# Kernel optimization log

Hardware: AMD Instinct MI355X
Metric: run time of the kernel (lower is better)

Reference implementation:

```python
import jax, jax.numpy as jnp
import numpy as np

N_NODES = 10000
N_EDGES = 160000
N_GRAPHS = 100
D = 32
E_DIM = 6
Q = 96
C = 2
EPS = 1e-5
S2S_STEPS = 3


def _bn(x, gamma, beta):
    # BatchNorm1d in training mode: normalize over the batch (row) axis
    mu = jnp.mean(x, axis=0)
    var = jnp.var(x, axis=0)
    return gamma * (x - mu) * jax.lax.rsqrt(var + EPS) + beta


def _mlp_layer(x, w, b, gamma, beta):
    # Linear -> ReLU -> BatchNorm1d (one block of the MLP helper)
    return _bn(jax.nn.relu(x @ w.T + b), gamma, beta)


def _nnconv(x, src, dst, edge_attr, nw, nb, ng, nbeta, root, bias):
    # edge MLP -> per-edge [D, D] weight matrices
    w = _mlp_layer(edge_attr, nw, nb, ng, nbeta).reshape(-1, D, D)  # [E, D, D]
    msg = jnp.einsum('ei,eio->eo', x[src], w)                       # per-edge matvec
    agg = jax.ops.segment_sum(msg, dst, num_segments=N_NODES)      # aggr='add'
    return agg + x @ root + bias                                    # root weight + bias


def _set2set(x, batch, w_ih, w_hh, b_ih, b_hh):
    h = jnp.zeros((N_GRAPHS, Q), x.dtype)
    c = jnp.zeros((N_GRAPHS, Q), x.dtype)
    q_star = jnp.zeros((N_GRAPHS, 2 * Q), x.dtype)
    for _ in range(S2S_STEPS):
        gates = q_star @ w_ih.T + b_ih + h @ w_hh.T + b_hh  # [B, 4Q], gate order i,f,g,o
        i, f, g, o = jnp.split(gates, 4, axis=1)
        c = jax.nn.sigmoid(f) * c + jax.nn.sigmoid(i) * jnp.tanh(g)
        h = jax.nn.sigmoid(o) * jnp.tanh(c)
        e = jnp.sum(x * h[batch], axis=-1)  # [N] attention logits
        emax = jax.ops.segment_max(e, batch, num_segments=N_GRAPHS)
        emax = jnp.where(jnp.isfinite(emax), emax, 0.0)
        a = jnp.exp(e - emax[batch])
        asum = jax.ops.segment_sum(a, batch, num_segments=N_GRAPHS)
        a = a / asum[batch]
        r = jax.ops.segment_sum(a[:, None] * x, batch, num_segments=N_GRAPHS)  # [B, Q]
        q_star = jnp.concatenate([h, r], axis=1)
    return q_star  # [B, 2Q]


def setup_inputs() -> dict:
    key = jax.random.key(0)
    ks = iter(jax.random.split(key, 48))
    def rn(shape, fan_in):
        return jax.random.normal(next(ks), shape, dtype=jnp.float32) * (1.0 / np.sqrt(fan_in))
    d = {}
    d['x'] = jax.random.normal(next(ks), (N_NODES, D), dtype=jnp.float32)
    d['edge_attr'] = jax.random.uniform(next(ks), (N_EDGES, E_DIM), dtype=jnp.float32)
    # conv1 edge-MLP + root + bias
    d['c1_nn_w'] = rn((D * D, E_DIM), E_DIM); d['c1_nn_b'] = jnp.zeros((D * D,), jnp.float32)
    d['c1_nn_g'] = jnp.ones((D * D,), jnp.float32); d['c1_nn_beta'] = jnp.zeros((D * D,), jnp.float32)
    d['c1_root'] = rn((D, D), D); d['c1_bias'] = jnp.zeros((D,), jnp.float32)
    # conv2
    d['c2_nn_w'] = rn((D * D, E_DIM), E_DIM); d['c2_nn_b'] = jnp.zeros((D * D,), jnp.float32)
    d['c2_nn_g'] = jnp.ones((D * D,), jnp.float32); d['c2_nn_beta'] = jnp.zeros((D * D,), jnp.float32)
    d['c2_root'] = rn((D, D), D); d['c2_bias'] = jnp.zeros((D,), jnp.float32)
    # lin1: MLP([2D, Q])
    d['lin1_w'] = rn((Q, 2 * D), 2 * D); d['lin1_b'] = jnp.zeros((Q,), jnp.float32)
    d['lin1_g'] = jnp.ones((Q,), jnp.float32); d['lin1_beta'] = jnp.zeros((Q,), jnp.float32)
    # Set2Set LSTM: input 2Q -> hidden Q
    d['lstm_w_ih'] = rn((4 * Q, 2 * Q), 2 * Q); d['lstm_w_hh'] = rn((4 * Q, Q), Q)
    d['lstm_b_ih'] = jnp.zeros((4 * Q,), jnp.float32); d['lstm_b_hh'] = jnp.zeros((4 * Q,), jnp.float32)
    # S2Slin: Linear(2Q, Q)
    d['s2s_w'] = rn((Q, 2 * Q), 2 * Q); d['s2s_b'] = jnp.zeros((Q,), jnp.float32)
    # mlp1: MLP([Q, Q, C])
    d['m1_w'] = rn((Q, Q), Q); d['m1_b'] = jnp.zeros((Q,), jnp.float32)
    d['m1_g'] = jnp.ones((Q,), jnp.float32); d['m1_beta'] = jnp.zeros((Q,), jnp.float32)
    d['m2_w'] = rn((C, Q), Q); d['m2_b'] = jnp.zeros((C,), jnp.float32)
    d['m2_g'] = jnp.ones((C,), jnp.float32); d['m2_beta'] = jnp.zeros((C,), jnp.float32)
    # graph structure
    d['edge_src'] = jax.random.randint(next(ks), (N_EDGES,), 0, N_NODES, dtype=jnp.int32)
    d['edge_dst'] = jax.random.randint(next(ks), (N_EDGES,), 0, N_NODES, dtype=jnp.int32)
    d['batch'] = jnp.sort(jax.random.randint(next(ks), (N_NODES,), 0, N_GRAPHS, dtype=jnp.int32))
    return d


def reference(x, edge_attr,
              c1_nn_w, c1_nn_b, c1_nn_g, c1_nn_beta, c1_root, c1_bias,
              c2_nn_w, c2_nn_b, c2_nn_g, c2_nn_beta, c2_root, c2_bias,
              lin1_w, lin1_b, lin1_g, lin1_beta,
              lstm_w_ih, lstm_w_hh, lstm_b_ih, lstm_b_hh,
              s2s_w, s2s_b,
              m1_w, m1_b, m1_g, m1_beta,
              m2_w, m2_b, m2_g, m2_beta,
              edge_src, edge_dst, batch):
    x1 = _nnconv(x, edge_src, edge_dst, edge_attr, c1_nn_w, c1_nn_b, c1_nn_g, c1_nn_beta, c1_root, c1_bias)
    x2 = _nnconv(x1, edge_src, edge_dst, edge_attr, c2_nn_w, c2_nn_b, c2_nn_g, c2_nn_beta, c2_root, c2_bias)
    xc = _mlp_layer(jnp.concatenate([x1, x2], axis=1), lin1_w, lin1_b, lin1_g, lin1_beta)  # [N, Q]
    qs = _set2set(xc, batch, lstm_w_ih, lstm_w_hh, lstm_b_ih, lstm_b_hh)                   # [B, 2Q]
    xg = qs @ s2s_w.T + s2s_b                                                               # [B, Q]
    xg = _mlp_layer(xg, m1_w, m1_b, m1_g, m1_beta)
    out = _mlp_layer(xg, m2_w, m2_b, m2_g, m2_beta)                                         # [B, C]
    return out
```

## Files before the change

### kernel.cpp

```cpp
#include <hip/hip_runtime.h>
#include <math.h>

#define NN 10000
#define NE 160000
#define NG 100
#define DD 32
#define QQ 96
#define EPS 1e-5f

typedef float f2 __attribute__((ext_vector_type(2)));

__global__ __launch_bounds__(512) void k_stats5(const float* __restrict__ ea,
        const float* __restrict__ w1, const float* __restrict__ b1,
        const float* __restrict__ w2, const float* __restrict__ b2,
        float* __restrict__ stats) {
    __shared__ float eas[1536];
    const int tid = threadIdx.x;
    const int chunk = blockIdx.x >> 1;
    const int ct = ((blockIdx.x & 1) << 9) | tid;
    const float* wr1 = w1 + ct * 6;
    const float* wr2 = w2 + ct * 6;
    f2 W0 = {wr1[0], wr2[0]}, W1 = {wr1[1], wr2[1]}, W2 = {wr1[2], wr2[2]};
    f2 W3 = {wr1[3], wr2[3]}, W4 = {wr1[4], wr2[4]}, W5 = {wr1[5], wr2[5]};
    f2 Bb = {b1[ct], b2[ct]};
    f2 S = {0.f, 0.f}, SS = {0.f, 0.f};
    const int base = chunk * 1536;
    eas[tid]        = ea[base + tid];
    eas[tid + 512]  = ea[base + tid + 512];
    eas[tid + 1024] = ea[base + tid + 1024];
    __syncthreads();
#pragma unroll 4
    for (int el = 0; el < 256; ++el) {
        const float* ep = &eas[el * 6];
        float2 p0 = *reinterpret_cast<const float2*>(ep);
        float2 p1 = *reinterpret_cast<const float2*>(ep + 2);
        float2 p2 = *reinterpret_cast<const float2*>(ep + 4);
        f2 y = Bb;
        y = p0.x * W0 + y;
        y = p0.y * W1 + y;
        y = p1.x * W2 + y;
        y = p1.y * W3 + y;
        y = p2.x * W4 + y;
        y = p2.y * W5 + y;
        f2 r = {fmaxf(y.x, 0.f), fmaxf(y.y, 0.f)};
        S = S + r;
        SS = r * r + SS;
    }
    atomicAdd(&stats[ct], S.x);
    atomicAdd(&stats[1024 + ct], SS.x);
    atomicAdd(&stats[2048 + ct], S.y);
    atomicAdd(&stats[3072 + ct], SS.y);
}

__global__ __launch_bounds__(256) void k_root(const float* __restrict__ x,
        const float* __restrict__ root, const float* __restrict__ bias,
        float* __restrict__ out,
        int doFin, const float* __restrict__ stats,
        const float* __restrict__ g1, const float* __restrict__ beta1,
        const float* __restrict__ g2, const float* __restrict__ beta2,
        const float* __restrict__ nw1, const float* __restrict__ nb1,
        const float* __restrict__ nw2, const float* __restrict__ nb2,
        float* __restrict__ wpack) {
    const int tid = threadIdx.x;
    if (doFin && blockIdx.x == gridDim.x - 1) {
        const float invE = 1.f / NE;
        for (int j = tid; j < 2048; j += 256) {
            int cv = j >> 10, col = j & 1023;
            const float* st = stats + cv * 2048;
            const float* g = cv ? g2 : g1;
            const float* bt = cv ? beta2 : beta1;
            const float* w = (cv ? nw2 : nw1) + col * 6;
            const float* nb = cv ? nb2 : nb1;
            float mean = st[col] * invE;
            float var = fmaxf(st[1024 + col] * invE - mean * mean, 0.f);
            float a = g[col] * rsqrtf(var + EPS);
            float b = bt[col] - mean * a;
            float* rec = wpack + cv * 12288 + col * 12;
            rec[0] = w[0]; rec[1] = w[1]; rec[2] = w[2];
            rec[3] = w[3]; rec[4] = w[4]; rec[5] = w[5];
            rec[6] = nb[col]; rec[7] = a; rec[8] = b;
        }
        return;
    }
    __shared__ float rlds[1024];
#pragma unroll
    for (int r = 0; r < 4; ++r) rlds[tid + 256 * r] = root[tid + 256 * r];
    __syncthreads();
    const int o = tid & 31;
    const int gg = tid >> 5;
    const int n = blockIdx.x * 8 + gg;
    if (n >= NN) return;
    const int half = tid & 32;
    float xs = x[n * 32 + o];
    float acc = bias[o];
#pragma unroll
    for (int i = 0; i < 32; ++i) {
        float xi = __shfl(xs, half | i);
        acc = fmaf(xi, rlds[i * 32 + o], acc);
    }
    out[n * 32 + o] = acc;
}

#define CDECL(K) float w##K##0, w##K##1, w##K##2, w##K##3, w##K##4, w##K##5, bs##K, av##K, bv##K;
#define CLOAD(K) { const int _j = (((w << 2) + (K << 1) + p) << 5) | o; \
    const float* _r = wp + _j * 12; \
    float4 _wa = *reinterpret_cast<const float4*>(_r); \
    float4 _wb = *reinterpret_cast<const float4*>(_r + 4); \
    w##K##0 = _wa.x; w##K##1 = _wa.y; w##K##2 = _wa.z; w##K##3 = _wa.w; \
    w##K##4 = _wb.x; w##K##5 = _wb.y; bs##K = _wb.z; av##K = _wb.w; \
    bv##K = _r[8]; }
#define CPIN(K) asm("" : "+v"(w##K##0), "+v"(w##K##1), "+v"(w##K##2), "+v"(w##K##3), \
                         "+v"(w##K##4), "+v"(w##K##5), "+v"(bs##K), "+v"(av##K), "+v"(bv##K));
#define CACC(K, XK, M) { float _y = bs##K; \
    _y = fmaf(e0, w##K##0, _y); _y = fmaf(e1, w##K##1, _y); _y = fmaf(e2, w##K##2, _y); \
    _y = fmaf(e3, w##K##3, _y); _y = fmaf(e4, w##K##4, _y); _y = fmaf(e5, w##K##5, _y); \
    float _t = fmaf(av##K, fmaxf(_y, 0.f), bv##K); M = fmaf(XK, _t, M); }

__global__ __launch_bounds__(512) void k_conv(const float* __restrict__ xin,
        const float* __restrict__ ea, const int* __restrict__ src, const int* __restrict__ dst,
        const float* __restrict__ wp, float* __restrict__ agg) {
    __shared__ float part[8][16][32];
    const int tid = threadIdx.x;
    const int lane = tid & 63;
    const int w = tid >> 6;
    const int p = lane >> 5;
    const int o = lane & 31;

    CDECL(0) CDECL(1)
    CLOAD(0) CLOAD(1)
    CPIN(0) CPIN(1)

    const int base0 = blockIdx.x * 80;
#pragma unroll 1
    for (int ch = 0; ch < 5; ++ch) {
        const int base = base0 + ch * 16;
#pragma unroll 4
        for (int m = 0; m < 16; ++m) {
            const int e = base + m;
            const int sc = src[e];
            const float* er = ea + e * 6;
            float e0 = er[0], e1 = er[1], e2 = er[2], e3 = er[3], e4 = er[4], e5 = er[5];
            float4 qa = *reinterpret_cast<const float4*>(xin + sc * 32 + (w << 2));
            float xA = p ? qa.y : qa.x;
            float xB = p ? qa.w : qa.z;
            float msg = 0.f;
            CACC(0, xA, msg) CACC(1, xB, msg)
            msg += __shfl_xor(msg, 32, 64);
            if (p == 0) part[w][m][o] = msg;
        }
        __syncthreads();
        {
            const int m = tid >> 5;
            const int e = base + m;
            const int dd = dst[e];
            float sum = part[0][m][o] + part[1][m][o] + part[2][m][o] + part[3][m][o]
                      + part[4][m][o] + part[5][m][o] + part[6][m][o] + part[7][m][o];
            atomicAdd(&agg[dd * 32 + o], sum);
        }
        __syncthreads();
    }
}

__global__ __launch_bounds__(384) void k_lin1a(const float* __restrict__ x1,
        const float* __restrict__ x2, const float* __restrict__ lw, const float* __restrict__ lb,
        float* __restrict__ pre, float* __restrict__ gsum, float* __restrict__ gsumsq) {
    __shared__ float cat[4][64];
    __shared__ float sh_s[96], sh_ss[96];
    const int tid = threadIdx.x;
    const int np = tid / 96;
    const int q = tid - np * 96;
    float w[64];
#pragma unroll
    for (int k = 0; k < 64; ++k) w[k] = lw[q * 64 + k];
    const float bq = lb[q];
    float s = 0.f, ss = 0.f;
    for (int nb = blockIdx.x * 4; nb < NN; nb += gridDim.x * 4) {
        __syncthreads();
        if (tid < 256) {
            int n2 = tid >> 6, k = tid & 63;
            cat[n2][k] = (k < 32) ? x1[(nb + n2) * 32 + k] : x2[(nb + n2) * 32 + (k - 32)];
        }
        __syncthreads();
        float v = bq;
#pragma unroll
        for (int k = 0; k < 64; ++k) v = fmaf(cat[np][k], w[k], v);
        float r = fmaxf(v, 0.f);
        pre[(nb + np) * 96 + q] = r;
        s += r; ss = fmaf(r, r, ss);
    }
    __syncthreads();
    if (tid < 96) { sh_s[tid] = 0.f; sh_ss[tid] = 0.f; }
    __syncthreads();
    atomicAdd(&sh_s[q], s);
    atomicAdd(&sh_ss[q], ss);
    __syncthreads();
    if (tid < 96) {
        atomicAdd(&gsum[tid], sh_s[tid]);
        atomicAdd(&gsumsq[tid], sh_ss[tid]);
    }
}

__global__ __launch_bounds__(512) void k_s2s(const float* __restrict__ pre,
        const int* __restrict__ batch,
        const float* __restrict__ gsum, const float* __restrict__ gsumsq,
        const float* __restrict__ lg, const float* __restrict__ lbeta,
        const float* __restrict__ w_ih, const float* __restrict__ w_hh,
        const float* __restrict__ b_ih, const float* __restrict__ b_hh,
        float* __restrict__ qs_g, float* __restrict__ e_ws) {
    __shared__ float qs[192], h[96], c[96], gates[384];
    __shared__ float ab_a[96], ab_b[96], hA[96], bh[96];
    __shared__ float redm[8], reds[8];
    __shared__ float racc_s[5][96];
    __shared__ float sh_scal[3];
    __shared__ int sse[2];
    const int tid = threadIdx.x;
    const int wid = tid >> 6, lane = tid & 63;
    const int b = blockIdx.x;
    if (tid < 2) {
        int key = b + tid, lo = 0, hi = NN;
        while (lo < hi) { int mid = (lo + hi) >> 1; if (batch[mid] < key) lo = mid + 1; else hi = mid; }
        sse[tid] = lo;
    }
    if (tid < 192) qs[tid] = 0.f;
    if (tid < 96) {
        h[tid] = 0.f; c[tid] = 0.f;
        const float invN = 1.f / NN;
        float mean = gsum[tid] * invN;
        float var = fmaxf(gsumsq[tid] * invN - mean * mean, 0.f);
        float a = lg[tid] * rsqrtf(var + EPS);
        ab_a[tid] = a;
        ab_b[tid] = lbeta[tid] - mean * a;
    }
    __syncthreads();
    const int s = sse[0], t = sse[1];
    for (int step = 0; step < 3; ++step) {
        if (tid < 384) {
            float acc = b_ih[tid] + b_hh[tid];
            const float* wi = &w_ih[tid * 192];
#pragma unroll 8
            for (int k = 0; k < 192; ++k) acc = fmaf(qs[k], wi[k], acc);
            const float* wh = &w_hh[tid * 96];
#pragma unroll 8
            for (int k = 0; k < 96; ++k) acc = fmaf(h[k], wh[k], acc);
            gates[tid] = acc;
        }
        __syncthreads();
        if (tid < 96) {
            float ig = 1.f / (1.f + __expf(-gates[tid]));
            float fg = 1.f / (1.f + __expf(-gates[96 + tid]));
            float gg = tanhf(gates[192 + tid]);
            float og = 1.f / (1.f + __expf(-gates[288 + tid]));
            float cn = fg * c[tid] + ig * gg;
            c[tid] = cn;
            float hn = og * tanhf(cn);
            h[tid] = hn;
            hA[tid] = ab_a[tid] * hn;
            bh[tid] = ab_b[tid] * hn;
        }
        __syncthreads();
        if (tid < 64) {
            float v = bh[tid] + (tid < 32 ? bh[64 + tid] : 0.f);
#pragma unroll
            for (int off = 32; off > 0; off >>= 1) v += __shfl_down(v, off);
            if (tid == 0) sh_scal[2] = v;
        }
        __syncthreads();
        const float hb = sh_scal[2];
        float pmax = -INFINITY;
        for (int n = s + tid; n < t; n += 512) {
            const float* xr = &pre[n * 96];
            float acc = hb;
#pragma unroll 8
            for (int k = 0; k < 96; ++k) acc = fmaf(xr[k], hA[k], acc);
            e_ws[n] = acc;
            pmax = fmaxf(pmax, acc);
        }
#pragma unroll
        for (int off = 32; off > 0; off >>= 1) pmax = fmaxf(pmax, __shfl_down(pmax, off));
        if (lane == 0) redm[wid] = pmax;
        __syncthreads();
        if (tid == 0) {
            float m = redm[0];
#pragma unroll
            for (int i = 1; i < 8; ++i) m = fmaxf(m, redm[i]);
            if (!isfinite(m)) m = 0.f;
            sh_scal[0] = m;
        }
        __syncthreads();
        const float emax = sh_scal[0];
        float pa = 0.f;
        for (int n = s + tid; n < t; n += 512) {
            float a = __expf(e_ws[n] - emax);
            e_ws[n] = a;
            pa += a;
        }
#pragma unroll
        for (int off = 32; off > 0; off >>= 1) pa += __shfl_down(pa, off);
        if (lane == 0) reds[wid] = pa;
        __syncthreads();
        if (tid == 0) {
            float a2 = 0.f;
#pragma unroll
            for (int i = 0; i < 8; ++i) a2 += reds[i];
            sh_scal[1] = (a2 > 0.f) ? 1.f / a2 : 0.f;
        }
        __syncthreads();
        const int g = tid / 96, q = tid - g * 96;
        if (tid < 480) {
            float racc = 0.f;
            for (int n = s + g; n < t; n += 5)
                racc = fmaf(e_ws[n], pre[n * 96 + q], racc);
            racc_s[g][q] = racc;
        }
        __syncthreads();
        if (tid < 96) {
            float inv = sh_scal[1];
            float racc5 = racc_s[0][tid] + racc_s[1][tid] + racc_s[2][tid]
                        + racc_s[3][tid] + racc_s[4][tid];
            float rq = (inv > 0.f) ? fmaf(ab_a[tid], racc5 * inv, ab_b[tid]) : 0.f;
            qs[tid] = h[tid];
            qs[96 + tid] = rq;
        }
        __syncthreads();
    }
    if (tid < 192) qs_g[b * 192 + tid] = qs[tid];
}

__global__ __launch_bounds__(128) void k_xg(const float* __restrict__ qs_g,
        const float* __restrict__ sw, const float* __restrict__ sb,
        const float* __restrict__ m1w, const float* __restrict__ m1b,
        float* __restrict__ pre, float* __restrict__ gsum, float* __restrict__ gsumsq) {
    __shared__ float xg0[96];
    const int tid = threadIdx.x;
    const int b = blockIdx.x;
    if (tid < 96) {
        const float* q = &qs_g[b * 192];
        float acc = sb[tid];
        const float* w = &sw[tid * 192];
#pragma unroll 8
        for (int k = 0; k < 192; ++k) acc = fmaf(q[k], w[k], acc);
        xg0[tid] = acc;
    }
    __syncthreads();
    if (tid < 96) {
        float acc = m1b[tid];
        const float* w = &m1w[tid * 96];
#pragma unroll 8
        for (int k = 0; k < 96; ++k) acc = fmaf(xg0[k], w[k], acc);
        float r = fmaxf(acc, 0.f);
        pre[b * 96 + tid] = r;
        atomicAdd(&gsum[tid], r);
        atomicAdd(&gsumsq[tid], r * r);
    }
}

__global__ __launch_bounds__(256) void k_tail(const float* __restrict__ pre,
        const float* __restrict__ gsum, const float* __restrict__ gsumsq,
        const float* __restrict__ g1, const float* __restrict__ beta1,
        const float* __restrict__ m2w, const float* __restrict__ m2b,
        const float* __restrict__ g2, const float* __restrict__ beta2,
        float* __restrict__ out) {
    __shared__ float xg1[100][97];
    __shared__ float pre2[200];
    __shared__ float ab2[4];
    const int tid = threadIdx.x;
    if (tid < 96) {
        const float invN = 1.f / NG;
        float mean = gsum[tid] * invN;
        float var = fmaxf(gsumsq[tid] * invN - mean * mean, 0.f);
        float a = g1[tid] * rsqrtf(var + EPS);
        float bb = beta1[tid] - mean * a;
        for (int n = 0; n < NG; ++n)
            xg1[n][tid] = fmaf(a, pre[n * 96 + tid], bb);
    }
    __syncthreads();
    if (tid < 200) {
        int n = tid >> 1, cc = tid & 1;
        float acc = m2b[cc];
        const float* w = &m2w[cc * 96];
#pragma unroll 8
        for (int k = 0; k < 96; ++k) acc = fmaf(xg1[n][k], w[k], acc);
        pre2[tid] = fmaxf(acc, 0.f);
    }
    __syncthreads();
    if (tid < 2) {
        float s = 0.f, ss = 0.f;
        for (int n = 0; n < NG; ++n) { float v = pre2[n * 2 + tid]; s += v; ss = fmaf(v, v, ss); }
        const float invN = 1.f / NG;
        float mean = s * invN;
        float var = fmaxf(ss * invN - mean * mean, 0.f);
        float a = g2[tid] * rsqrtf(var + EPS);
        ab2[tid] = a;
        ab2[2 + tid] = beta2[tid] - mean * a;
    }
    __syncthreads();
    if (tid < 200) {
        int cc = tid & 1;
        out[tid] = fmaf(ab2[cc], pre2[tid], ab2[2 + cc]);
    }
}

extern "C" void kernel_launch(void* const* d_in, const int* in_sizes, int n_in,
                              void* d_out, int out_size, void* d_ws, size_t ws_size,
                              hipStream_t stream) {
    (void)in_sizes; (void)n_in; (void)out_size; (void)ws_size;
    const float* x       = (const float*)d_in[0];
    const float* ea      = (const float*)d_in[1];
    const float* c1w     = (const float*)d_in[2];
    const float* c1b     = (const float*)d_in[3];
    const float* c1g     = (const float*)d_in[4];
    const float* c1beta  = (const float*)d_in[5];
    const float* c1root  = (const float*)d_in[6];
    const float* c1bias  = (const float*)d_in[7];
    const float* c2w     = (const float*)d_in[8];
    const float* c2b     = (const float*)d_in[9];
    const float* c2g     = (const float*)d_in[10];
    const float* c2beta  = (const float*)d_in[11];
    const float* c2root  = (const float*)d_in[12];
    const float* c2bias  = (const float*)d_in[13];
    const float* lin1w   = (const float*)d_in[14];
    const float* lin1b   = (const float*)d_in[15];
    const float* lin1g   = (const float*)d_in[16];
    const float* lin1bt  = (const float*)d_in[17];
    const float* wih     = (const float*)d_in[18];
    const float* whh     = (const float*)d_in[19];
    const float* bih     = (const float*)d_in[20];
    const float* bhh     = (const float*)d_in[21];
    const float* s2sw    = (const float*)d_in[22];
    const float* s2sb    = (const float*)d_in[23];
    const float* m1w     = (const float*)d_in[24];
    const float* m1b     = (const float*)d_in[25];
    const float* m1g     = (const float*)d_in[26];
    const float* m1beta  = (const float*)d_in[27];
    const float* m2w     = (const float*)d_in[28];
    const float* m2b     = (const float*)d_in[29];
    const float* m2g     = (const float*)d_in[30];
    const float* m2beta  = (const float*)d_in[31];
    const int* src       = (const int*)d_in[32];
    const int* dst       = (const int*)d_in[33];
    const int* batch     = (const int*)d_in[34];

    float* ws = (float*)d_ws;
    float* stats  = ws;
    float* linst  = ws + 8192;
    float* m1st   = ws + 8384;
    float* wpack  = ws + 8704;
    float* x1     = wpack + 24576;
    float* x2     = x1 + 320000;
    float* prelin = x2 + 320000;
    float* e_ws   = prelin + 960000;
    float* qs_g   = e_ws + 10000;
    float* prem1  = qs_g + 19200;

    hipMemsetAsync(ws, 0, 8576 * sizeof(float), stream);

    k_stats5<<<1250, 512, 0, stream>>>(ea, c1w, c1b, c2w, c2b, stats);

    k_root<<<1251, 256, 0, stream>>>(x, c1root, c1bias, x1,
                                     1, stats, c1g, c1beta, c2g, c2beta,
                                     c1w, c1b, c2w, c2b, wpack);
    k_conv<<<2000, 512, 0, stream>>>(x, ea, src, dst, wpack, x1);

    k_root<<<1250, 256, 0, stream>>>(x1, c2root, c2bias, x2,
                                     0, stats, c1g, c1beta, c2g, c2beta,
                                     c1w, c1b, c2w, c2b, wpack);
    k_conv<<<2000, 512, 0, stream>>>(x1, ea, src, dst, wpack + 12288, x2);

    k_lin1a<<<500, 384, 0, stream>>>(x1, x2, lin1w, lin1b, prelin, linst, linst + 96);

    k_s2s<<<100, 512, 0, stream>>>(prelin, batch, linst, linst + 96, lin1g, lin1bt,
                                   wih, whh, bih, bhh, qs_g, e_ws);

    k_xg<<<100, 128, 0, stream>>>(qs_g, s2sw, s2sb, m1w, m1b, prem1, m1st, m1st + 96);
    k_tail<<<1, 256, 0, stream>>>(prem1, m1st, m1st + 96, m1g, m1beta,
                                  m2w, m2b, m2g, m2beta, (float*)d_out);
}
```

Measured before the change: 318.6 us.

## Pack edge-MLP weights as fp16 records and halve conv block width

The edge-network weight records are now split into a 16-byte record (three half2 weight pairs plus an fp32 bias) and an 8-byte BN scale/shift pair. k_conv no longer pins these in registers. Each lane now handles four output columns and reloads the records from memory for every edge, and the block shrinks to 256 threads with four waves. This trades register pressure and block size for repeated per-edge weight loads, which should hit in cache, and it adds fp16 rounding to the edge MLP weights, a small accuracy risk.

```diff
diff --git a/kernel.cpp b/kernel.cpp
--- a/kernel.cpp
+++ b/kernel.cpp
@@ -1,4 +1,5 @@
 #include <hip/hip_runtime.h>
+#include <hip/hip_fp16.h>
 #include <math.h>
 
 #define NN 10000
@@ -60,7 +61,7 @@
         const float* __restrict__ g2, const float* __restrict__ beta2,
         const float* __restrict__ nw1, const float* __restrict__ nb1,
         const float* __restrict__ nw2, const float* __restrict__ nb2,
-        float* __restrict__ wpack) {
+        uint4* __restrict__ recA, float2* __restrict__ recB) {
     const int tid = threadIdx.x;
     if (doFin && blockIdx.x == gridDim.x - 1) {
         const float invE = 1.f / NE;
@@ -75,10 +76,16 @@
             float var = fmaxf(st[1024 + col] * invE - mean * mean, 0.f);
             float a = g[col] * rsqrtf(var + EPS);
             float b = bt[col] - mean * a;
-            float* rec = wpack + cv * 12288 + col * 12;
-            rec[0] = w[0]; rec[1] = w[1]; rec[2] = w[2];
-            rec[3] = w[3]; rec[4] = w[4]; rec[5] = w[5];
-            rec[6] = nb[col]; rec[7] = a; rec[8] = b;
+            __half2 h01 = __floats2half2_rn(w[0], w[1]);
+            __half2 h23 = __floats2half2_rn(w[2], w[3]);
+            __half2 h45 = __floats2half2_rn(w[4], w[5]);
+            uint4 ra;
+            ra.x = *reinterpret_cast<unsigned int*>(&h01);
+            ra.y = *reinterpret_cast<unsigned int*>(&h23);
+            ra.z = *reinterpret_cast<unsigned int*>(&h45);
+            ra.w = __float_as_uint(nb[col]);
+            recA[j] = ra;
+            recB[j] = make_float2(a, b);
         }
         return;
     }
@@ -101,34 +108,32 @@
     out[n * 32 + o] = acc;
 }
 
-#define CDECL(K) float w##K##0, w##K##1, w##K##2, w##K##3, w##K##4, w##K##5, bs##K, av##K, bv##K;
-#define CLOAD(K) { const int _j = (((w << 2) + (K << 1) + p) << 5) | o; \
-    const float* _r = wp + _j * 12; \
-    float4 _wa = *reinterpret_cast<const float4*>(_r); \
-    float4 _wb = *reinterpret_cast<const float4*>(_r + 4); \
-    w##K##0 = _wa.x; w##K##1 = _wa.y; w##K##2 = _wa.z; w##K##3 = _wa.w; \
-    w##K##4 = _wb.x; w##K##5 = _wb.y; bs##K = _wb.z; av##K = _wb.w; \
-    bv##K = _r[8]; }
-#define CPIN(K) asm("" : "+v"(w##K##0), "+v"(w##K##1), "+v"(w##K##2), "+v"(w##K##3), \
-                         "+v"(w##K##4), "+v"(w##K##5), "+v"(bs##K), "+v"(av##K), "+v"(bv##K));
-#define CACC(K, XK, M) { float _y = bs##K; \
-    _y = fmaf(e0, w##K##0, _y); _y = fmaf(e1, w##K##1, _y); _y = fmaf(e2, w##K##2, _y); \
-    _y = fmaf(e3, w##K##3, _y); _y = fmaf(e4, w##K##4, _y); _y = fmaf(e5, w##K##5, _y); \
-    float _t = fmaf(av##K, fmaxf(_y, 0.f), bv##K); M = fmaf(XK, _t, M); }
-
-__global__ __launch_bounds__(512) void k_conv(const float* __restrict__ xin,
+#define CACCH(J, XK, M) { \
+    uint4 _ra = wa[J]; float2 _rb = wb[J]; \
+    __half2 _h01 = *reinterpret_cast<const __half2*>(&_ra.x); \
+    __half2 _h23 = *reinterpret_cast<const __half2*>(&_ra.y); \
+    __half2 _h45 = *reinterpret_cast<const __half2*>(&_ra.z); \
+    float _y = __uint_as_float(_ra.w); \
+    _y = fmaf(e0, __low2float(_h01), _y); _y = fmaf(e1, __high2float(_h01), _y); \
+    _y = fmaf(e2, __low2float(_h23), _y); _y = fmaf(e3, __high2float(_h23), _y); \
+    _y = fmaf(e4, __low2float(_h45), _y); _y = fmaf(e5, __high2float(_h45), _y); \
+    float _t = fmaf(_rb.x, fmaxf(_y, 0.f), _rb.y); M = fmaf(XK, _t, M); }
+
+__global__ __launch_bounds__(256) void k_conv(const float* __restrict__ xin,
         const float* __restrict__ ea, const int* __restrict__ src, const int* __restrict__ dst,
-        const float* __restrict__ wp, float* __restrict__ agg) {
-    __shared__ float part[8][16][32];
+        const uint4* __restrict__ wa, const float2* __restrict__ wb,
+        float* __restrict__ agg) {
+    __shared__ float part[4][16][32];
     const int tid = threadIdx.x;
     const int lane = tid & 63;
     const int w = tid >> 6;
     const int p = lane >> 5;
     const int o = lane & 31;
 
-    CDECL(0) CDECL(1)
-    CLOAD(0) CLOAD(1)
-    CPIN(0) CPIN(1)
+    const int j0 = (((w << 3) + 0 + p) << 5) | o;
+    const int j1 = (((w << 3) + 2 + p) << 5) | o;
+    const int j2 = (((w << 3) + 4 + p) << 5) | o;
+    const int j3 = (((w << 3) + 6 + p) << 5) | o;
 
     const int base0 = blockIdx.x * 80;
 #pragma unroll 1
@@ -140,11 +145,13 @@
             const int sc = src[e];
             const float* er = ea + e * 6;
             float e0 = er[0], e1 = er[1], e2 = er[2], e3 = er[3], e4 = er[4], e5 = er[5];
-            float4 qa = *reinterpret_cast<const float4*>(xin + sc * 32 + (w << 2));
-            float xA = p ? qa.y : qa.x;
-            float xB = p ? qa.w : qa.z;
+            const float* xr = xin + sc * 32 + (w << 3);
+            float4 qa = *reinterpret_cast<const float4*>(xr);
+            float4 qb = *reinterpret_cast<const float4*>(xr + 4);
+            float xA = p ? qa.y : qa.x, xB = p ? qa.w : qa.z;
+            float xC = p ? qb.y : qb.x, xD = p ? qb.w : qb.z;
             float msg = 0.f;
-            CACC(0, xA, msg) CACC(1, xB, msg)
+            CACCH(j0, xA, msg) CACCH(j1, xB, msg) CACCH(j2, xC, msg) CACCH(j3, xD, msg)
             msg += __shfl_xor(msg, 32, 64);
             if (p == 0) part[w][m][o] = msg;
         }
@@ -153,9 +160,13 @@
             const int m = tid >> 5;
             const int e = base + m;
             const int dd = dst[e];
-            float sum = part[0][m][o] + part[1][m][o] + part[2][m][o] + part[3][m][o]
-                      + part[4][m][o] + part[5][m][o] + part[6][m][o] + part[7][m][o];
+            float sum = part[0][m][o] + part[1][m][o] + part[2][m][o] + part[3][m][o];
             atomicAdd(&agg[dd * 32 + o], sum);
+            const int m2 = m + 8;
+            const int e2 = base + m2;
+            const int dd2 = dst[e2];
+            float sum2 = part[0][m2][o] + part[1][m2][o] + part[2][m2][o] + part[3][m2][o];
+            atomicAdd(&agg[dd2 * 32 + o], sum2);
         }
         __syncthreads();
     }
@@ -444,8 +455,9 @@
     float* stats  = ws;
     float* linst  = ws + 8192;
     float* m1st   = ws + 8384;
-    float* wpack  = ws + 8704;
-    float* x1     = wpack + 24576;
+    uint4*  recA  = (uint4*)(ws + 8704);
+    float2* recB  = (float2*)(ws + 16896);
+    float* x1     = ws + 20992;
     float* x2     = x1 + 320000;
     float* prelin = x2 + 320000;
     float* e_ws   = prelin + 960000;
@@ -458,13 +470,13 @@
 
     k_root<<<1251, 256, 0, stream>>>(x, c1root, c1bias, x1,
                                      1, stats, c1g, c1beta, c2g, c2beta,
-                                     c1w, c1b, c2w, c2b, wpack);
-    k_conv<<<2000, 512, 0, stream>>>(x, ea, src, dst, wpack, x1);
+                                     c1w, c1b, c2w, c2b, recA, recB);
+    k_conv<<<2000, 256, 0, stream>>>(x, ea, src, dst, recA, recB, x1);
 
     k_root<<<1250, 256, 0, stream>>>(x1, c2root, c2bias, x2,
                                      0, stats, c1g, c1beta, c2g, c2beta,
-                                     c1w, c1b, c2w, c2b, wpack);
-    k_conv<<<2000, 512, 0, stream>>>(x1, ea, src, dst, wpack + 12288, x2);
+                                     c1w, c1b, c2w, c2b, recA, recB);
+    k_conv<<<2000, 256, 0, stream>>>(x1, ea, src, dst, recA + 1024, recB + 1024, x2);
 
     k_lin1a<<<500, 384, 0, stream>>>(x1, x2, lin1w, lin1b, prelin, linst, linst + 96);
 
```

Result: faster. 290.8 us (-8.7%).
